# Kernel tuning notes

Hardware: AMD Instinct MI355X
Metric: run time of the kernel (lower is better)

Reference implementation:

```python
import math
import jax, jax.numpy as jnp
import numpy as np

# Neuron / simulation constants (from docstring defaults)
THETA = 10.0
TAU_SR = 10.0
TAU_REF = 1.0
SCALE_REF = 2.0
SCALE_RHO = 1.0
TS = 1.0
T_SAMPLE = 300


def _alpha_kernel(tau, mult, eps_tol):
    # Faithful to slayer._calculateAlphaKernel: eps(t) = mult * t/tau * exp(1 - t/tau),
    # truncated once |eps| < eps_tol and t > tau.
    vals = []
    for t in np.arange(0.0, T_SAMPLE, TS):
        v = mult * t / tau * math.exp(1.0 - t / tau)
        if abs(v) < eps_tol and t > tau:
            break
        vals.append(v)
    return np.asarray(vals, np.float32)


def psp(spike, srm_kernel):
    # slayerCuda.conv: causal temporal convolution psp[t] = sum_k f[k] * spike[t-k]
    N, C, H, W, T = spike.shape
    x = spike.reshape(-1, 1, T)                       # (B,1,T), B = N*C*H*W
    K = srm_kernel.shape[0]
    w = jnp.flip(srm_kernel).reshape(1, 1, K).astype(x.dtype)
    y = jax.lax.conv_general_dilated(
        x, w, window_strides=(1,), padding=[(K - 1, 0)],
        dimension_numbers=('NCH', 'OIH', 'NCH'))
    return y.reshape(N, C, H, W, T)


def get_spikes(u2, ref_kernel):
    # slayerCuda.getSpikes: sequential scan over time. At each step the effective
    # membrane potential is u[t] plus pending refractory contributions from past
    # spikes; a spike (value 1/Ts) fires when u_eff >= theta and injects the
    # refractory kernel into future timesteps.
    # u2: (B, T); ref_kernel: (K,) with ref_kernel[0] == 0 (alpha kernel).
    B, T = u2.shape
    K = ref_kernel.shape[0]
    ref_tail = ref_kernel[1:].astype(u2.dtype)        # contributions to t+1..t+K-1

    def step(pend, u_t):
        u_eff = u_t + pend[:, 0]
        s = (u_eff >= THETA).astype(u2.dtype)
        pend = jnp.concatenate([pend[:, 1:], jnp.zeros_like(pend[:, :1])], axis=1)
        pend = pend + s[:, None] * ref_tail[None, :]
        return pend, (s / TS, u_eff)

    pend0 = jnp.zeros((B, K - 1), u2.dtype)
    _, (s, u_mod) = jax.lax.scan(step, pend0, u2.T)
    return s.T, u_mod.T


def setup_inputs() -> dict:
    key = jax.random.key(0)
    k1, = jax.random.split(key, 1)
    N, C, H, W, T = 4, 16, 32, 32, T_SAMPLE
    u = jax.random.uniform(k1, (N, C, H, W, T), dtype=jnp.float32)
    spike_in = (u < 0.05).astype(jnp.float32) / TS
    srm_kernel = jnp.asarray(_alpha_kernel(TAU_SR, 1.0, 0.01))
    ref_kernel = jnp.asarray(_alpha_kernel(TAU_REF, -SCALE_REF * THETA, 0.01))
    return {"spike_in": spike_in, "srm_kernel": srm_kernel, "ref_kernel": ref_kernel}


def reference(spike_in, srm_kernel, ref_kernel):
    # psp (exponential alpha PSP conv) followed by spike generation scan
    u = psp(spike_in, srm_kernel)                     # (N,C,H,W,T)
    T = u.shape[-1]
    s, _ = get_spikes(u.reshape(-1, T), ref_kernel)
    return s.reshape(spike_in.shape)
```

## Files before the change

### kernel.cpp

```cpp
#include <hip/hip_runtime.h>


#define T_LEN 300
#define CH 20
#define NCHUNK 15
#define KS 77
#define KR 10
#define THETA_V 10.0f
#define TSZ 115

#define RHO_F   0.9048374180359596f
#define C_E10   0.2718281828459045f
#define THR_D   (9.0f / C_E10)
#define TAP_TOL 2e-3f

__global__ __launch_bounds__(256) void pack_zero_kernel(
    const float* __restrict__ spike_in, unsigned* __restrict__ packed,
    float* __restrict__ out, long long N, long long ngroups)
{
    const int lane = threadIdx.x & 63;
    const long long wid = (long long)blockIdx.x * (blockDim.x >> 6) + (threadIdx.x >> 6);
    const long long nw  = (long long)gridDim.x * (blockDim.x >> 6);
    const long long gtid = (long long)blockIdx.x * blockDim.x + threadIdx.x;
    const long long nthr = (long long)gridDim.x * blockDim.x;

    if (gtid < 4) packed[gtid] = 0u;

    for (long long g = wid; g < ngroups; g += nw) {
        const long long f = g * 64 + lane;
        float x = (f < N) ? spike_in[f] : 0.0f;
        unsigned long long m = __ballot(x != 0.0f);
        if (lane == 0) packed[4 + 2 * g]     = (unsigned)m;
        if (lane == 1) packed[4 + 2 * g + 1] = (unsigned)(m >> 32);
    }

    const float4 z = make_float4(0.0f, 0.0f, 0.0f, 0.0f);
    float4* o4 = (float4*)out;
    const long long nf4 = N >> 2;
    for (long long i = gtid; i < nf4; i += nthr) o4[i] = z;
}

__global__ __launch_bounds__(256) void flag_kernel(
    const unsigned* __restrict__ packed,
    const float* __restrict__ srm, int srm_len,
    unsigned* __restrict__ flags, int B)
{
    const int n = blockIdx.x * blockDim.x + threadIdx.x;
    if (n >= B) return;

    bool ok = (srm_len == KS);
    if (ok) {
        ok = fabsf(srm[0]) <= TAP_TOL;
        float pj = 1.0f;
        for (int j = 1; j < KS; ++j) {
            pj *= RHO_F;
            float mj = C_E10 * (float)j * pj;
            ok = ok && (fabsf(srm[j] - mj) <= TAP_TOL);
        }
    }

    const long long F0 = 300LL * n;
    const int q = 4 + (int)(F0 >> 5);
    const int r = (int)(F0 & 31);
    unsigned W[11];
#pragma unroll
    for (int k = 0; k < 11; ++k) W[k] = packed[q + k];
    unsigned aw[10];
#pragma unroll
    for (int k = 0; k < 10; ++k)
        aw[k] = (unsigned)((((unsigned long long)W[k + 1] << 32) | W[k]) >> r);

    float A = 0.0f, D = 0.0f, dmax = 0.0f;
#pragma unroll
    for (int t = 1; t < T_LEN; ++t) {
        const int bw = (t - 1) >> 5;
        const int bb = (t - 1) & 31;
        int ms = ((int)(aw[bw] << (31 - bb))) >> 31;
        float xr = __int_as_float(ms & __float_as_int(RHO_F));
        A = fmaf(RHO_F, A, xr);
        D = fmaf(RHO_F, D, A);
        dmax = fmaxf(dmax, D);
    }

    flags[n] = (!ok || (dmax >= THR_D)) ? 1u : 0u;
}

__global__ __launch_bounds__(256) void scan_fix_kernel(
    const float* __restrict__ spike_in,
    const float* __restrict__ srm, int srm_len,
    const float* __restrict__ refk, int ref_len,
    float* __restrict__ out, const unsigned* __restrict__ flags, int B)
{
    __shared__ float T[TSZ + 13];
    {
        int k = threadIdx.x;
        if (k < TSZ + 13) {
            int j = k - 19;
            T[k] = (j >= 1 && j < KS && j < srm_len) ? srm[j] : 0.0f;
        }
    }
    __syncthreads();

    int b = blockIdx.x * blockDim.x + threadIdx.x;
    if (b >= B) return;
    if (flags[b] == 0u) return;

    const float* row  = spike_in + (size_t)b * T_LEN;
    float*       orow = out      + (size_t)b * T_LEN;

    float rt[KR];
#pragma unroll
    for (int i = 0; i < KR; ++i) rt[i] = (i + 1 < ref_len) ? refk[i + 1] : 0.0f;
    float pend[KR];
#pragma unroll
    for (int i = 0; i < KR; ++i) pend[i] = 0.0f;

    unsigned w0 = 0, w1 = 0, w2 = 0;
    float nxt[CH];
    {
        const float4* p = (const float4*)row;
#pragma unroll
        for (int i = 0; i < CH / 4; ++i) {
            float4 v = p[i];
            nxt[4*i+0] = v.x; nxt[4*i+1] = v.y; nxt[4*i+2] = v.z; nxt[4*i+3] = v.w;
        }
    }

#pragma unroll 1
    for (int ch = 0; ch < NCHUNK; ++ch) {
        unsigned nb = 0;
#pragma unroll
        for (int i = 0; i < CH; ++i)
            nb |= (nxt[i] != 0.0f) ? (1u << i) : 0u;

        w0 = (w0 >> 20) | (w1 << 12);
        w1 = (w1 >> 20) | (w2 << 12);
        w2 = (w2 >> 20) | (nb << 12);

        if (ch + 1 < NCHUNK) {
            const float4* p = (const float4*)(row + (ch + 1) * CH);
#pragma unroll
            for (int i = 0; i < CH / 4; ++i) {
                float4 v = p[i];
                nxt[4*i+0] = v.x; nxt[4*i+1] = v.y; nxt[4*i+2] = v.z; nxt[4*i+3] = v.w;
            }
        }
        __builtin_amdgcn_sched_barrier(0);

        float u[CH];
#pragma unroll
        for (int c = 0; c < CH; ++c) u[c] = 0.0f;

        unsigned a0 = w0, a1 = w1, a2 = w2;
        while (__ballot(a0 | a1 | a2)) {
            int p = a2 ? (95 - __clz(a2))
                       : (a1 ? (63 - __clz(a1))
                             : (a0 ? (31 - __clz(a0)) : 95));
            unsigned m = 1u << (p & 31);
            if (p >= 64)      a2 &= ~m;
            else if (p >= 32) a1 &= ~m;
            else              a0 &= ~m;

            const float* tp = &T[95 - p];
#pragma unroll
            for (int c = 0; c < CH; ++c)
                u[c] += tp[c];
        }

        float so[CH];
#pragma unroll
        for (int c = 0; c < CH; ++c) {
            const int r = c % KR;
            float u_eff = u[c] + pend[r];
            float s = (u_eff >= THETA_V) ? 1.0f : 0.0f;
#pragma unroll
            for (int i = 0; i < KR - 1; ++i)
                pend[(r + 1 + i) % KR] = fmaf(s, rt[i], pend[(r + 1 + i) % KR]);
            pend[r] = s * rt[KR - 1];
            so[c] = s;
        }

        float4* op = (float4*)(orow + ch * CH);
#pragma unroll
        for (int i = 0; i < CH / 4; ++i) {
            float4 v;
            v.x = so[4*i+0]; v.y = so[4*i+1]; v.z = so[4*i+2]; v.w = so[4*i+3];
            op[i] = v;
        }
    }
}

__global__ __launch_bounds__(256)
__attribute__((amdgpu_waves_per_eu(1, 1)))
void spike_layer_kernel(
    const float* __restrict__ spike_in,
    const float* __restrict__ srm, int srm_len,
    const float* __restrict__ refk, int ref_len,
    float* __restrict__ out, int B)
{
    __shared__ float T[TSZ + 13];
    {
        int k = threadIdx.x;
        if (k < TSZ + 13) {
            int j = k - 19;
            T[k] = (j >= 1 && j < KS && j < srm_len) ? srm[j] : 0.0f;
        }
    }
    __syncthreads();

    int b = blockIdx.x * blockDim.x + threadIdx.x;
    if (b >= B) return;

    const float* row  = spike_in + (size_t)b * T_LEN;
    float*       orow = out      + (size_t)b * T_LEN;

    float rt[KR];
#pragma unroll
    for (int i = 0; i < KR; ++i) rt[i] = (i + 1 < ref_len) ? refk[i + 1] : 0.0f;
    float pend[KR];
#pragma unroll
    for (int i = 0; i < KR; ++i) pend[i] = 0.0f;

    unsigned w0 = 0, w1 = 0, w2 = 0;
    float nxt[CH];
    {
        const float4* p = (const float4*)row;
#pragma unroll
        for (int i = 0; i < CH / 4; ++i) {
            float4 v = p[i];
            nxt[4*i+0] = v.x; nxt[4*i+1] = v.y; nxt[4*i+2] = v.z; nxt[4*i+3] = v.w;
        }
    }

#pragma unroll 1
    for (int ch = 0; ch < NCHUNK; ++ch) {
        unsigned nb = 0;
#pragma unroll
        for (int i = 0; i < CH; ++i)
            nb |= (nxt[i] != 0.0f) ? (1u << i) : 0u;

        w0 = (w0 >> 20) | (w1 << 12);
        w1 = (w1 >> 20) | (w2 << 12);
        w2 = (w2 >> 20) | (nb << 12);

        if (ch + 1 < NCHUNK) {
            const float4* p = (const float4*)(row + (ch + 1) * CH);
#pragma unroll
            for (int i = 0; i < CH / 4; ++i) {
                float4 v = p[i];
                nxt[4*i+0] = v.x; nxt[4*i+1] = v.y; nxt[4*i+2] = v.z; nxt[4*i+3] = v.w;
            }
        }
        __builtin_amdgcn_sched_barrier(0);

        float u[CH];
#pragma unroll
        for (int c = 0; c < CH; ++c) u[c] = 0.0f;

        unsigned a0 = w0, a1 = w1, a2 = w2;
        while (__ballot(a0 | a1 | a2)) {
            int p = a2 ? (95 - __clz(a2))
                       : (a1 ? (63 - __clz(a1))
                             : (a0 ? (31 - __clz(a0)) : 95));
            unsigned m = 1u << (p & 31);
            if (p >= 64)      a2 &= ~m;
            else if (p >= 32) a1 &= ~m;
            else              a0 &= ~m;

            const float* tp = &T[95 - p];
#pragma unroll
            for (int c = 0; c < CH; ++c)
                u[c] += tp[c];
        }

        float so[CH];
#pragma unroll
        for (int c = 0; c < CH; ++c) {
            const int r = c % KR;
            float u_eff = u[c] + pend[r];
            float s = (u_eff >= THETA_V) ? 1.0f : 0.0f;
#pragma unroll
            for (int i = 0; i < KR - 1; ++i)
                pend[(r + 1 + i) % KR] = fmaf(s, rt[i], pend[(r + 1 + i) % KR]);
            pend[r] = s * rt[KR - 1];
            so[c] = s;
        }

        float4* op = (float4*)(orow + ch * CH);
#pragma unroll
        for (int i = 0; i < CH / 4; ++i) {
            float4 v;
            v.x = so[4*i+0]; v.y = so[4*i+1]; v.z = so[4*i+2]; v.w = so[4*i+3];
            op[i] = v;
        }
    }
}

extern "C" void kernel_launch(void* const* d_in, const int* in_sizes, int n_in,
                              void* d_out, int out_size, void* d_ws, size_t ws_size,
                              hipStream_t stream) {
    const float* spike_in = (const float*)d_in[0];
    const float* srm      = (const float*)d_in[1];
    const float* refk     = (const float*)d_in[2];
    float* out = (float*)d_out;

    int srm_len = in_sizes[1];
    int ref_len = in_sizes[2];
    int B = in_sizes[0] / T_LEN;

    const long long N = (long long)B * T_LEN;
    const long long ngroups = (N + 63) / 64;
    const long long packed_words = 4 + 2 * ngroups + 2;
    const size_t need = (size_t)(packed_words + B) * sizeof(unsigned);

    if (d_ws != nullptr && ws_size >= need) {
        unsigned* packed = (unsigned*)d_ws;
        unsigned* flags  = packed + packed_words;
        pack_zero_kernel<<<2048, 256, 0, stream>>>(spike_in, packed, out,
                                                   N, ngroups);
        flag_kernel<<<(B + 255) / 256, 256, 0, stream>>>(packed, srm, srm_len,
                                                         flags, B);
        scan_fix_kernel<<<(B + 255) / 256, 256, 0, stream>>>(
            spike_in, srm, srm_len, refk, ref_len, out, flags, B);
    } else {
        int grid = (B + 255) / 256;
        spike_layer_kernel<<<grid, 256, 0, stream>>>(spike_in, srm, srm_len,
                                                     refk, ref_len, out, B);
    }
}
```

Before: 160.8 us.

## Fuse spike bit-packing, output zeroing and flag computation into one kernel

Merges the pack/zero kernel and the flag kernel into a single kernel where each block packs the spike bits for 64 neurons into shared memory, zeroes its slice of the output, then computes the per-neuron flags from LDS. This removes one kernel launch and the global round-trip of the packed bit array. In exchange only 64 of 256 threads run the serial flag scan, so each block has low utilisation during that phase. There are also fewer blocks (B/64, 1024 for this input) than the previous 2048-block pack grid.

After: 149.9 us. 6.8% less time.

```diff
diff --git a/kernel.cpp b/kernel.cpp
--- a/kernel.cpp
+++ b/kernel.cpp
@@ -14,75 +14,106 @@
 #define THR_D   (9.0f / C_E10)
 #define TAP_TOL 2e-3f
 
-__global__ __launch_bounds__(256) void pack_zero_kernel(
-    const float* __restrict__ spike_in, unsigned* __restrict__ packed,
-    float* __restrict__ out, long long N, long long ngroups)
+#define NPB  64
+#define WPG  600
+#define F4PG 4800
+
+__global__ __launch_bounds__(256) void fused_kernel(
+    const float* __restrict__ spike_in,
+    const float* __restrict__ srm, int srm_len,
+    float* __restrict__ out, unsigned* __restrict__ flags, int B)
 {
-    const int lane = threadIdx.x & 63;
-    const long long wid = (long long)blockIdx.x * (blockDim.x >> 6) + (threadIdx.x >> 6);
-    const long long nw  = (long long)gridDim.x * (blockDim.x >> 6);
-    const long long gtid = (long long)blockIdx.x * blockDim.x + threadIdx.x;
-    const long long nthr = (long long)gridDim.x * blockDim.x;
-
-    if (gtid < 4) packed[gtid] = 0u;
-
-    for (long long g = wid; g < ngroups; g += nw) {
-        const long long f = g * 64 + lane;
-        float x = (f < N) ? spike_in[f] : 0.0f;
-        unsigned long long m = __ballot(x != 0.0f);
-        if (lane == 0) packed[4 + 2 * g]     = (unsigned)m;
-        if (lane == 1) packed[4 + 2 * g + 1] = (unsigned)(m >> 32);
-    }
-
-    const float4 z = make_float4(0.0f, 0.0f, 0.0f, 0.0f);
-    float4* o4 = (float4*)out;
-    const long long nf4 = N >> 2;
-    for (long long i = gtid; i < nf4; i += nthr) o4[i] = z;
-}
-
-__global__ __launch_bounds__(256) void flag_kernel(
-    const unsigned* __restrict__ packed,
-    const float* __restrict__ srm, int srm_len,
-    unsigned* __restrict__ flags, int B)
-{
-    const int n = blockIdx.x * blockDim.x + threadIdx.x;
-    if (n >= B) return;
-
-    bool ok = (srm_len == KS);
-    if (ok) {
-        ok = fabsf(srm[0]) <= TAP_TOL;
-        float pj = 1.0f;
-        for (int j = 1; j < KS; ++j) {
-            pj *= RHO_F;
-            float mj = C_E10 * (float)j * pj;
-            ok = ok && (fabsf(srm[j] - mj) <= TAP_TOL);
-        }
-    }
-
-    const long long F0 = 300LL * n;
-    const int q = 4 + (int)(F0 >> 5);
-    const int r = (int)(F0 & 31);
-    unsigned W[11];
-#pragma unroll
-    for (int k = 0; k < 11; ++k) W[k] = packed[q + k];
-    unsigned aw[10];
-#pragma unroll
-    for (int k = 0; k < 10; ++k)
-        aw[k] = (unsigned)((((unsigned long long)W[k + 1] << 32) | W[k]) >> r);
-
-    float A = 0.0f, D = 0.0f, dmax = 0.0f;
-#pragma unroll
-    for (int t = 1; t < T_LEN; ++t) {
-        const int bw = (t - 1) >> 5;
-        const int bb = (t - 1) & 31;
-        int ms = ((int)(aw[bw] << (31 - bb))) >> 31;
-        float xr = __int_as_float(ms & __float_as_int(RHO_F));
-        A = fmaf(RHO_F, A, xr);
-        D = fmaf(RHO_F, D, A);
-        dmax = fmaxf(dmax, D);
-    }
-
-    flags[n] = (!ok || (dmax >= THR_D)) ? 1u : 0u;
+    __shared__ unsigned Wlds[WPG + 8];
+
+    const int t = threadIdx.x;
+    const int g = blockIdx.x;
+    const long long NF     = (long long)B * T_LEN;
+    const long long base_f = (long long)NPB * T_LEN * g;
+
+#pragma unroll
+    for (int k = 0; k < 3; ++k) {
+        const int w = t + 256 * k;
+        if (w < WPG) {
+            const long long f0 = base_f + 32LL * w;
+            unsigned bits = 0u;
+            if (f0 + 32 <= NF) {
+                const float4* p = (const float4*)(spike_in + f0);
+#pragma unroll
+                for (int i = 0; i < 8; ++i) {
+                    float4 v = p[i];
+                    bits |= (v.x != 0.0f ? 1u : 0u) << (4 * i + 0);
+                    bits |= (v.y != 0.0f ? 1u : 0u) << (4 * i + 1);
+                    bits |= (v.z != 0.0f ? 1u : 0u) << (4 * i + 2);
+                    bits |= (v.w != 0.0f ? 1u : 0u) << (4 * i + 3);
+                }
+            } else {
+                for (int j = 0; j < 32; ++j) {
+                    const long long f = f0 + j;
+                    float x = (f < NF) ? spike_in[f] : 0.0f;
+                    bits |= (x != 0.0f ? 1u : 0u) << j;
+                }
+            }
+            Wlds[w] = bits;
+        }
+    }
+    if (t < 8) Wlds[WPG + t] = 0u;
+
+    {
+        const float4 z = make_float4(0.0f, 0.0f, 0.0f, 0.0f);
+        const long long nf4 = NF >> 2;
+        float4* o4 = (float4*)out;
+#pragma unroll
+        for (int k = 0; k < 19; ++k) {
+            const int lw = t + 256 * k;
+            if (lw < F4PG) {
+                const long long i4 = (long long)F4PG * g + lw;
+                if (i4 < nf4) o4[i4] = z;
+            }
+        }
+    }
+
+    __syncthreads();
+
+    if (t < NPB) {
+        const long long neuron = (long long)NPB * g + t;
+        if (neuron < B) {
+            bool ok = (srm_len == KS);
+            if (ok) {
+                ok = fabsf(srm[0]) <= TAP_TOL;
+                float pj = 1.0f;
+                for (int j = 1; j < KS; ++j) {
+                    pj *= RHO_F;
+                    float mj = C_E10 * (float)j * pj;
+                    ok = ok && (fabsf(srm[j] - mj) <= TAP_TOL);
+                }
+            }
+
+            const int F0 = T_LEN * t;
+            const int q = F0 >> 5;
+            const int r = F0 & 31;
+            unsigned W[11];
+#pragma unroll
+            for (int k = 0; k < 11; ++k) W[k] = Wlds[q + k];
+            unsigned aw[10];
+#pragma unroll
+            for (int k = 0; k < 10; ++k)
+                aw[k] = (unsigned)((((unsigned long long)W[k + 1] << 32) | W[k]) >> r);
+
+            float A = 0.0f, D = 0.0f, dmax = 0.0f;
+#pragma unroll
+            for (int tt = 1; tt < T_LEN; ++tt) {
+                const int bw = (tt - 1) >> 5;
+                const int bb = (tt - 1) & 31;
+                int ms = ((int)(aw[bw] << (31 - bb))) >> 31;
+                float xr = __int_as_float(ms & __float_as_int(RHO_F));
+                A = fmaf(RHO_F, A, xr);
+                D = fmaf(RHO_F, D, A);
+                dmax = fmaxf(dmax, D);
+            }
+
+            flags[neuron] = (!ok || (dmax >= THR_D)) ? 1u : 0u;
+        }
+    }
 }
 
 __global__ __launch_bounds__(256) void scan_fix_kernel(
@@ -308,18 +339,13 @@
     int ref_len = in_sizes[2];
     int B = in_sizes[0] / T_LEN;
 
-    const long long N = (long long)B * T_LEN;
-    const long long ngroups = (N + 63) / 64;
-    const long long packed_words = 4 + 2 * ngroups + 2;
-    const size_t need = (size_t)(packed_words + B) * sizeof(unsigned);
+    const size_t need = (size_t)B * sizeof(unsigned);
 
     if (d_ws != nullptr && ws_size >= need) {
-        unsigned* packed = (unsigned*)d_ws;
-        unsigned* flags  = packed + packed_words;
-        pack_zero_kernel<<<2048, 256, 0, stream>>>(spike_in, packed, out,
-                                                   N, ngroups);
-        flag_kernel<<<(B + 255) / 256, 256, 0, stream>>>(packed, srm, srm_len,
-                                                         flags, B);
+        unsigned* flags = (unsigned*)d_ws;
+        const int groups = (B + NPB - 1) / NPB;
+        fused_kernel<<<groups, 256, 0, stream>>>(spike_in, srm, srm_len,
+                                                 out, flags, B);
         scan_fix_kernel<<<(B + 255) / 256, 256, 0, stream>>>(
             spike_in, srm, srm_len, refk, ref_len, out, flags, B);
     } else {
```
